# Performance work log

Hardware: AMD Instinct MI355X
Metric: run time of the kernel (lower is better)

Reference implementation:

```python
import jax, jax.numpy as jnp
import numpy as np

TAU_SYN_INV = 0.5
TAU_MEM_INV = 0.5
V_TH = 1.0
V_RESET = 0.0
INHIBITION_STRENGTH = -5.0

B, N = 4096, 8192


def setup_inputs() -> dict:
    key = jax.random.key(0)
    kx, kv, ki = jax.random.split(key, 3)
    x = jax.random.normal(kx, (B, N), dtype=jnp.float32)
    v = jax.random.uniform(kv, (B, N), dtype=jnp.float32)  # membrane potential state
    i = jax.random.normal(ki, (B, N), dtype=jnp.float32)   # synaptic current state
    return {"x": x, "v": v, "i": i}


def reference(x, v, i):
    # --- LIF step (custom_lif_step) ---
    i_new = i + TAU_SYN_INV * (x - i)
    v_new = v + TAU_MEM_INV * (i_new - v)
    z = (v_new >= V_TH).astype(v_new.dtype)            # spikes [B, N]
    v_before_reset = v_new
    v_after = jnp.where(z > 0, V_RESET, v_new)         # reset spiked neurons

    # --- lateral inhibition: per-row winner-take-all among spiked neurons ---
    # masked argmax over pre-reset potential; rows with no spikes are untouched
    scores = jnp.where(z > 0, v_before_reset, -jnp.inf)  # [B, N]
    winner = jnp.argmax(scores, axis=1)                  # [B], first max like torch
    any_spike = jnp.any(z > 0, axis=1)                   # [B]
    is_winner = winner[:, None] == jnp.arange(x.shape[1])[None, :]  # [B, N] bool

    v_out = jnp.where(
        any_spike[:, None],
        jnp.where(is_winner, v_after, INHIBITION_STRENGTH),
        v_after,
    )
    # forward returns (z, new_state); new_state = (z, v_out, i_new)
    return z, v_out, i_new
```

## Files before the change

### kernel.cpp

```cpp
#include <hip/hip_runtime.h>


constexpr int B = 4096;
constexpr int N = 8192;
constexpr int BLOCK = 256;
constexpr int CHUNKS = N / (BLOCK * 4);

#define NEG_FLT_MAX (-3.402823466e38f)

__device__ __forceinline__ void combine_argmax(float& bv, int& bi, float ov, int oi) {
    if (ov > bv || (ov == bv && oi < bi)) { bv = ov; bi = oi; }
}

__global__ __launch_bounds__(BLOCK) void lif_wta_kernel(
    const float* __restrict__ x_in,
    const float* __restrict__ v_in,
    const float* __restrict__ i_in,
    float* __restrict__ z_out,
    float* __restrict__ v_out,
    float* __restrict__ i_out)
{
    const int row = blockIdx.x;
    const int tid = threadIdx.x;
    const size_t base = (size_t)row * N;

    const float4* x4 = reinterpret_cast<const float4*>(x_in + base);
    const float4* v4 = reinterpret_cast<const float4*>(v_in + base);
    const float4* c4 = reinterpret_cast<const float4*>(i_in + base);
    float4* z4 = reinterpret_cast<float4*>(z_out + base);
    float4* o4 = reinterpret_cast<float4*>(v_out + base);
    float4* i4 = reinterpret_cast<float4*>(i_out + base);

    float4 vn[CHUNKS];
    float best_val = NEG_FLT_MAX;
    int   best_idx = 0x7fffffff;

#pragma unroll
    for (int k = 0; k < CHUNKS; ++k) {
        const int c = tid + k * BLOCK;
        const float4 xx = x4[c];
        const float4 vv = v4[c];
        const float4 ii = c4[c];
        float4 in4, zz;
        const int e0 = c * 4;

#define LIF_ELEM(f, j)                                                            \
        {                                                                         \
            float inew = __fadd_rn(ii.f, __fmul_rn(0.5f, __fsub_rn(xx.f, ii.f))); \
            float vnew = __fadd_rn(vv.f, __fmul_rn(0.5f, __fsub_rn(inew, vv.f))); \
            in4.f = inew;                                                         \
            vn[k].f = vnew;                                                       \
            if (vnew >= 1.0f) {                                                   \
                zz.f = 1.0f;                                                      \
                              \
                if (vnew > best_val) { best_val = vnew; best_idx = e0 + (j); }    \
            } else {                                                             \
                zz.f = 0.0f;                                                      \
            }                                                                     \
        }
        LIF_ELEM(x, 0)
        LIF_ELEM(y, 1)
        LIF_ELEM(z, 2)
        LIF_ELEM(w, 3)
#undef LIF_ELEM

        z4[c] = zz;
        i4[c] = in4;
    }

#pragma unroll
    for (int off = 32; off > 0; off >>= 1) {
        float ov = __shfl_down(best_val, off);
        int   oi = __shfl_down(best_idx, off);
        combine_argmax(best_val, best_idx, ov, oi);
    }

    __shared__ float s_val[BLOCK / 64];
    __shared__ int   s_idx[BLOCK / 64];
    __shared__ float s_bval;
    __shared__ int   s_bidx;

    const int wave = tid >> 6;
    const int lane = tid & 63;
    if (lane == 0) { s_val[wave] = best_val; s_idx[wave] = best_idx; }
    __syncthreads();
    if (tid == 0) {
        float bv = s_val[0]; int bi = s_idx[0];
#pragma unroll
        for (int w = 1; w < BLOCK / 64; ++w) combine_argmax(bv, bi, s_val[w], s_idx[w]);
        s_bval = bv; s_bidx = bi;
    }
    __syncthreads();
    const float row_best = s_bval;
    const int   winner   = s_bidx;

    if (row_best >= 1.0f) {
#pragma unroll
        for (int k = 0; k < CHUNKS; ++k) {
            const int c = tid + k * BLOCK;
            const int e0 = c * 4;
            float4 o;
            o.x = (e0     == winner) ? 0.0f : -5.0f;
            o.y = (e0 + 1 == winner) ? 0.0f : -5.0f;
            o.z = (e0 + 2 == winner) ? 0.0f : -5.0f;
            o.w = (e0 + 3 == winner) ? 0.0f : -5.0f;
            o4[c] = o;
        }
    } else {
#pragma unroll
        for (int k = 0; k < CHUNKS; ++k) {
            o4[tid + k * BLOCK] = vn[k];
        }
    }
}

extern "C" void kernel_launch(void* const* d_in, const int* in_sizes, int n_in,
                              void* d_out, int out_size, void* d_ws, size_t ws_size,
                              hipStream_t stream) {
    const float* x = (const float*)d_in[0];
    const float* v = (const float*)d_in[1];
    const float* i = (const float*)d_in[2];

    float* out   = (float*)d_out;
    float* z_out = out;
    float* v_out = out + (size_t)B * N;
    float* i_out = out + 2 * (size_t)B * N;

    lif_wta_kernel<<<B, BLOCK, 0, stream>>>(x, v, i, z_out, v_out, i_out);
}
```

Baseline: 634.2 us.

## Recompute v_new instead of holding it in registers, add nontemporal stores

The per-thread array of eight float4 v_new values is no longer kept in registers across the row reduction. In the rare no-spike branch, x, v and i are re-read and v_new is recomputed. Together with launch bounds of 8 blocks and a partial unroll, this lowers register pressure so more waves can be resident to hide memory latency. All output stores become nontemporal to avoid polluting the cache. The cost is extra global reads for rows with no spikes, and possibly less instruction-level parallelism from the reduced unroll.

```diff
diff --git a/kernel.cpp b/kernel.cpp
--- a/kernel.cpp
+++ b/kernel.cpp
@@ -6,13 +6,22 @@
 constexpr int BLOCK = 256;
 constexpr int CHUNKS = N / (BLOCK * 4);
 
+typedef float fx4 __attribute__((ext_vector_type(4)));
+
 #define NEG_FLT_MAX (-3.402823466e38f)
 
 __device__ __forceinline__ void combine_argmax(float& bv, int& bi, float ov, int oi) {
     if (ov > bv || (ov == bv && oi < bi)) { bv = ov; bi = oi; }
 }
 
-__global__ __launch_bounds__(BLOCK) void lif_wta_kernel(
+__device__ __forceinline__ float lif_inew(float x, float i) {
+    return __fadd_rn(i, __fmul_rn(0.5f, __fsub_rn(x, i)));
+}
+__device__ __forceinline__ float lif_vnew(float v, float inew) {
+    return __fadd_rn(v, __fmul_rn(0.5f, __fsub_rn(inew, v)));
+}
+
+__global__ __launch_bounds__(BLOCK, 8) void lif_wta_kernel(
     const float* __restrict__ x_in,
     const float* __restrict__ v_in,
     const float* __restrict__ i_in,
@@ -24,48 +33,38 @@
     const int tid = threadIdx.x;
     const size_t base = (size_t)row * N;
 
-    const float4* x4 = reinterpret_cast<const float4*>(x_in + base);
-    const float4* v4 = reinterpret_cast<const float4*>(v_in + base);
-    const float4* c4 = reinterpret_cast<const float4*>(i_in + base);
-    float4* z4 = reinterpret_cast<float4*>(z_out + base);
-    float4* o4 = reinterpret_cast<float4*>(v_out + base);
-    float4* i4 = reinterpret_cast<float4*>(i_out + base);
+    const fx4* x4 = reinterpret_cast<const fx4*>(x_in + base);
+    const fx4* v4 = reinterpret_cast<const fx4*>(v_in + base);
+    const fx4* c4 = reinterpret_cast<const fx4*>(i_in + base);
+    fx4* z4 = reinterpret_cast<fx4*>(z_out + base);
+    fx4* o4 = reinterpret_cast<fx4*>(v_out + base);
+    fx4* i4 = reinterpret_cast<fx4*>(i_out + base);
 
-    float4 vn[CHUNKS];
     float best_val = NEG_FLT_MAX;
     int   best_idx = 0x7fffffff;
 
-#pragma unroll
+#pragma unroll 2
     for (int k = 0; k < CHUNKS; ++k) {
         const int c = tid + k * BLOCK;
-        const float4 xx = x4[c];
-        const float4 vv = v4[c];
-        const float4 ii = c4[c];
-        float4 in4, zz;
+        const fx4 xx = x4[c];
+        const fx4 vv = v4[c];
+        const fx4 ii = c4[c];
+        fx4 in4, zz;
         const int e0 = c * 4;
 
-#define LIF_ELEM(f, j)                                                            \
-        {                                                                         \
-            float inew = __fadd_rn(ii.f, __fmul_rn(0.5f, __fsub_rn(xx.f, ii.f))); \
-            float vnew = __fadd_rn(vv.f, __fmul_rn(0.5f, __fsub_rn(inew, vv.f))); \
-            in4.f = inew;                                                         \
-            vn[k].f = vnew;                                                       \
-            if (vnew >= 1.0f) {                                                   \
-                zz.f = 1.0f;                                                      \
-                              \
-                if (vnew > best_val) { best_val = vnew; best_idx = e0 + (j); }    \
-            } else {                                                             \
-                zz.f = 0.0f;                                                      \
-            }                                                                     \
+#pragma unroll
+        for (int j = 0; j < 4; ++j) {
+            float inew = lif_inew(xx[j], ii[j]);
+            float vnew = lif_vnew(vv[j], inew);
+            in4[j] = inew;
+            zz[j] = (vnew >= 1.0f) ? 1.0f : 0.0f;
+            if (vnew >= 1.0f && vnew > best_val) {
+                best_val = vnew; best_idx = e0 + j;
+            }
         }
-        LIF_ELEM(x, 0)
-        LIF_ELEM(y, 1)
-        LIF_ELEM(z, 2)
-        LIF_ELEM(w, 3)
-#undef LIF_ELEM
 
-        z4[c] = zz;
-        i4[c] = in4;
+        __builtin_nontemporal_store(zz, &z4[c]);
+        __builtin_nontemporal_store(in4, &i4[c]);
     }
 
 #pragma unroll
@@ -95,21 +94,28 @@
     const int   winner   = s_bidx;
 
     if (row_best >= 1.0f) {
-#pragma unroll
+#pragma unroll 2
         for (int k = 0; k < CHUNKS; ++k) {
             const int c = tid + k * BLOCK;
             const int e0 = c * 4;
-            float4 o;
-            o.x = (e0     == winner) ? 0.0f : -5.0f;
-            o.y = (e0 + 1 == winner) ? 0.0f : -5.0f;
-            o.z = (e0 + 2 == winner) ? 0.0f : -5.0f;
-            o.w = (e0 + 3 == winner) ? 0.0f : -5.0f;
-            o4[c] = o;
+            fx4 o;
+#pragma unroll
+            for (int j = 0; j < 4; ++j)
+                o[j] = (e0 + j == winner) ? 0.0f : -5.0f;
+            __builtin_nontemporal_store(o, &o4[c]);
         }
     } else {
+#pragma unroll 2
+        for (int k = 0; k < CHUNKS; ++k) {
+            const int c = tid + k * BLOCK;
+            const fx4 xx = x4[c];
+            const fx4 vv = v4[c];
+            const fx4 ii = c4[c];
+            fx4 o;
 #pragma unroll
-        for (int k = 0; k < CHUNKS; ++k) {
-            o4[tid + k * BLOCK] = vn[k];
+            for (int j = 0; j < 4; ++j)
+                o[j] = lif_vnew(vv[j], lif_inew(xx[j], ii[j]));
+            __builtin_nontemporal_store(o, &o4[c]);
         }
     }
 }
```

After: 651.7 us. 2.8% more time.
